# Performance work log

Hardware: AMD Instinct MI355X
Metric: run time of the kernel (lower is better)

Reference implementation:

```python
import jax, jax.numpy as jnp
import numpy as np

N_NODES = 50000
N_EDGES = 800000
D_IN = 96
D_OUT = 96


def setup_inputs() -> dict:
    key = jax.random.key(0)
    k1, k2, k3, k4 = jax.random.split(key, 4)
    feat = jax.random.normal(k1, (N_NODES, D_IN), dtype=jnp.float32)
    # xavier_normal-like init for weight, zeros bias (as in the torch module)
    std = (2.0 / (D_IN + D_OUT)) ** 0.5
    weight = jax.random.normal(k2, (D_IN, D_OUT), dtype=jnp.float32) * std
    bias = jnp.zeros((D_OUT,), dtype=jnp.float32)
    src = jax.random.randint(k3, (N_EDGES,), 0, N_NODES, dtype=jnp.int64)
    dst = jax.random.randint(k4, (N_EDGES,), 0, N_NODES, dtype=jnp.int64)
    return {"feat": feat, "weight": weight, "bias": bias, "src": src, "dst": dst}


def reference(feat, weight, bias, src, dst):
    N = feat.shape[0]
    ones = jnp.ones(src.shape[0], dtype=feat.dtype)
    out_deg = jax.ops.segment_sum(ones, src, num_segments=N)  # out-degree per node
    in_deg = jax.ops.segment_sum(ones, dst, num_segments=N)   # in-degree per node
    ci = jnp.clip(out_deg, 1.0, None) ** -0.5                 # src-side norm
    cj = jnp.clip(in_deg, 1.0, None) ** -0.5                  # dst-side norm
    # gather src features * ci, scatter-sum to dst, scale by cj
    msg = feat[src] * ci[src, None]                           # [E, D_IN]
    agg = jax.ops.segment_sum(msg, dst, num_segments=N) * cj[:, None]
    # DGL UDF reduce only updates nodes that receive messages; isolated
    # (zero in-degree) nodes keep their original features.
    h = jnp.where(in_deg[:, None] > 0, agg, feat)
    return jnp.matmul(h, weight) + bias
```

## Files before the change

kernel.cpp:

```cpp
#include <hip/hip_runtime.h>

#define N_NODES 50000
#define N_EDGES 800000
#define D 96
#define D4 (D / 4)

#define HB 128
#define CHUNK (N_EDGES / HB)
#define NW (N_NODES / 4)

#define RL 12
#define NTILES (N_NODES / 16)
#define CONV_BLOCKS ((N_NODES * RL + 255) / 256)
#define WPREP_BLOCKS ((D * (D / 2) + 255) / 256)

typedef __attribute__((ext_vector_type(8))) short short8;
typedef __attribute__((ext_vector_type(4))) float floatx4;

__device__ __forceinline__ short8 as_short8(uint4 u) { return *(short8*)&u; }

__global__ void __launch_bounds__(1024) hist_kernel(
        const int* __restrict__ src, const int* __restrict__ dst,
        unsigned* __restrict__ hist, unsigned* __restrict__ total) {
    __shared__ unsigned hbin[NW];
    int b = blockIdx.x, t = threadIdx.x;
    if (b == 0 && t == 0) *total = 0;
    int e0 = b * CHUNK;
#pragma unroll 1
    for (int p = 0; p < 2; ++p) {
        const int* __restrict__ arr = (p == 0) ? src : dst;
        for (int i = t; i < NW; i += 1024) hbin[i] = 0;
        __syncthreads();
        for (int i = t; i < CHUNK; i += 1024) {
            int l = arr[e0 + i];
            atomicAdd(&hbin[l >> 2], 1u << ((l & 3) * 8));
        }
        __syncthreads();
        unsigned* __restrict__ g = hist + ((size_t)p * HB + b) * NW;
        for (int i = t; i < NW; i += 1024) g[i] = hbin[i];
        __syncthreads();
    }
}

__global__ void __launch_bounds__(256) reduce_kernel(
        unsigned* __restrict__ hist, float* __restrict__ ci,
        int* __restrict__ deg_in, int* __restrict__ off,
        unsigned* __restrict__ total) {
    int w = blockIdx.x * 256 + threadIdx.x;
    bool valid = w < NW;
    unsigned acc_s = 0;
    int4 dv = {0, 0, 0, 0};
    if (valid) {
        const unsigned* __restrict__ ps = hist + w;
        unsigned* __restrict__ pd = hist + (size_t)HB * NW + w;
#pragma unroll 8
        for (int b = 0; b < HB; ++b) acc_s += ps[(size_t)b * NW];
        unsigned run = 0;
#pragma unroll 4
        for (int b = 0; b < HB; ++b) {
            unsigned v = pd[(size_t)b * NW];
            pd[(size_t)b * NW] = run;
            run += v;
        }
        dv.x = (int)( run        & 0xFFu);
        dv.y = (int)((run >>  8) & 0xFFu);
        dv.z = (int)((run >> 16) & 0xFFu);
        dv.w = (int)( run >> 24        );
    }
    int sum4 = dv.x + dv.y + dv.z + dv.w;
    int lane = threadIdx.x & 63;
    int incl = sum4;
#pragma unroll
    for (int st = 1; st < 64; st <<= 1) {
        int v = __shfl_up(incl, st, 64);
        if (lane >= st) incl += v;
    }
    int excl = incl - sum4;
    int wave_total = __shfl(incl, 63, 64);
    int base = 0;
    if (lane == 63) base = (int)atomicAdd(total, (unsigned)wave_total);
    base = __shfl(base, 63, 64);
    if (valid) {
        int n0 = 4 * w;
        int b0 = base + excl;
        int4 ov;
        ov.x = b0;
        ov.y = b0 + dv.x;
        ov.z = b0 + dv.x + dv.y;
        ov.w = b0 + dv.x + dv.y + dv.z;
        *(int4*)&off[n0] = ov;
        *(int4*)&deg_in[n0] = dv;
        float4 cv;
        cv.x = rsqrtf(fmaxf((float)( acc_s        & 0xFFu), 1.0f));
        cv.y = rsqrtf(fmaxf((float)((acc_s >>  8) & 0xFFu), 1.0f));
        cv.z = rsqrtf(fmaxf((float)((acc_s >> 16) & 0xFFu), 1.0f));
        cv.w = rsqrtf(fmaxf((float)( acc_s >> 24        ), 1.0f));
        *(float4*)&ci[n0] = cv;
    }
}

__device__ __forceinline__ unsigned bf16pack(float a, float b) {
    unsigned ua = __float_as_uint(a);
    unsigned ub = __float_as_uint(b);
    ua = (ua + 0x7FFFu + ((ua >> 16) & 1u)) >> 16;
    ub = (ub + 0x7FFFu + ((ub >> 16) & 1u)) & 0xFFFF0000u;
    return ua | ub;
}

__global__ void __launch_bounds__(256) conv_kernel(
        const float4* __restrict__ feat4, const float* __restrict__ ci,
        uint4* __restrict__ sfeat, const float* __restrict__ W,
        unsigned* __restrict__ WT32) {
    int blk = blockIdx.x;
    if (blk >= CONV_BLOCKS) {
        int t = (blk - CONV_BLOCKS) * 256 + threadIdx.x;
        if (t >= D * (D / 2)) return;
        int n = t / (D / 2);
        int j = t - n * (D / 2);
        float w0 = W[(2 * j) * D + n];
        float w1 = W[(2 * j + 1) * D + n];
        WT32[n * (D / 2) + j] = bf16pack(w0, w1);
        return;
    }
    int t = blk * 256 + threadIdx.x;
    if (t >= N_NODES * RL) return;
    int n = t / RL;
    int lane = t - n * RL;
    float c = ci[n];
    float4 a = feat4[n * D4 + lane * 2];
    float4 b = feat4[n * D4 + lane * 2 + 1];
    uint4 o;
    o.x = bf16pack(a.x * c, a.y * c);
    o.y = bf16pack(a.z * c, a.w * c);
    o.z = bf16pack(b.x * c, b.y * c);
    o.w = bf16pack(b.z * c, b.w * c);
    sfeat[t] = o;
}

__global__ void __launch_bounds__(1024) fill_kernel(
        const int* __restrict__ src, const int* __restrict__ dst,
        const int* __restrict__ off, const unsigned* __restrict__ hist,
        int* __restrict__ csr) {
    __shared__ unsigned cur[NW];
    int b = blockIdx.x, t = threadIdx.x;
    const unsigned* __restrict__ pr = hist + ((size_t)HB + b) * NW;
    for (int i = t; i < NW; i += 1024) cur[i] = pr[i];
    __syncthreads();
    int e0 = b * CHUNK;
    for (int i = t; i < CHUNK; i += 1024) {
        int d = dst[e0 + i];
        int sh = (d & 3) * 8;
        unsigned old = atomicAdd(&cur[d >> 2], 1u << sh);
        int pos = (int)((old >> sh) & 0xFFu);
        csr[off[d] + pos] = src[e0 + i];
    }
}

__global__ void __launch_bounds__(192) gather_kernel(
        const float4* __restrict__ feat4, const uint4* __restrict__ sfeat,
        const int* __restrict__ deg_in, const int* __restrict__ off,
        const int* __restrict__ csr, uint4* __restrict__ hbuf) {
    int tid = threadIdx.x;
    int g = tid / RL;
    int lane = tid - g * RL;
    int n = blockIdx.x * 16 + g;
    int deg = deg_in[n];
    uint4* __restrict__ hout = hbuf + (size_t)n * RL + lane;
    if (deg == 0) {
        float4 a = feat4[n * D4 + lane * 2];
        float4 b = feat4[n * D4 + lane * 2 + 1];
        uint4 o;
        o.x = bf16pack(a.x, a.y);
        o.y = bf16pack(a.z, a.w);
        o.z = bf16pack(b.x, b.y);
        o.w = bf16pack(b.z, b.w);
        *hout = o;
        return;
    }
    const int* bk = csr + off[n];
    const uint4* __restrict__ sf = sfeat + lane;
    float acc[8] = {};
#define ACC8(v)  { \
    acc[0] += __uint_as_float((v).x << 16); \
    acc[1] += __uint_as_float((v).x & 0xFFFF0000u); \
    acc[2] += __uint_as_float((v).y << 16); \
    acc[3] += __uint_as_float((v).y & 0xFFFF0000u); \
    acc[4] += __uint_as_float((v).z << 16); \
    acc[5] += __uint_as_float((v).z & 0xFFFF0000u); \
    acc[6] += __uint_as_float((v).w << 16); \
    acc[7] += __uint_as_float((v).w & 0xFFFF0000u); }
    int i = 0;
    for (; i + 3 < deg; i += 4) {
        int s0 = bk[i], s1 = bk[i + 1], s2 = bk[i + 2], s3 = bk[i + 3];
        uint4 v0 = sf[(size_t)s0 * RL];
        uint4 v1 = sf[(size_t)s1 * RL];
        uint4 v2 = sf[(size_t)s2 * RL];
        uint4 v3 = sf[(size_t)s3 * RL];
        ACC8(v0); ACC8(v1); ACC8(v2); ACC8(v3);
    }
    for (; i < deg; ++i) {
        uint4 v = sf[(size_t)bk[i] * RL];
        ACC8(v);
    }
#undef ACC8
    float cj = rsqrtf((float)deg);
    uint4 o;
    o.x = bf16pack(acc[0] * cj, acc[1] * cj);
    o.y = bf16pack(acc[2] * cj, acc[3] * cj);
    o.z = bf16pack(acc[4] * cj, acc[5] * cj);
    o.w = bf16pack(acc[6] * cj, acc[7] * cj);
    *hout = o;
}

__global__ void __launch_bounds__(256) mfma_mm_kernel(
        const uint4* __restrict__ hb4, const uint4* __restrict__ wt4,
        const float* __restrict__ bias, float* __restrict__ out) {
    int wave = threadIdx.x >> 6;
    int lane = threadIdx.x & 63;
    int tile = blockIdx.x * 4 + wave;
    if (tile >= NTILES) return;
    int m = lane & 15, quad = lane >> 4;
    int row0 = tile * 16;
    int rb = (row0 + m) * RL + quad;
    short8 a0 = as_short8(hb4[rb]);
    short8 a1 = as_short8(hb4[rb + 4]);
    short8 a2 = as_short8(hb4[rb + 8]);
    int r_out0 = row0 + quad * 4;
#pragma unroll
    for (int ct = 0; ct < 6; ++ct) {
        int n = ct * 16 + m;
        int wb = n * RL + quad;
        short8 b0 = as_short8(wt4[wb]);
        short8 b1 = as_short8(wt4[wb + 4]);
        short8 b2 = as_short8(wt4[wb + 8]);
        floatx4 c = {0.f, 0.f, 0.f, 0.f};
        c = __builtin_amdgcn_mfma_f32_16x16x32_bf16(a0, b0, c, 0, 0, 0);
        c = __builtin_amdgcn_mfma_f32_16x16x32_bf16(a1, b1, c, 0, 0, 0);
        c = __builtin_amdgcn_mfma_f32_16x16x32_bf16(a2, b2, c, 0, 0, 0);
        float bs = bias[n];
#pragma unroll
        for (int r = 0; r < 4; ++r)
            out[(size_t)(r_out0 + r) * D + n] = c[r] + bs;
    }
}

extern "C" void kernel_launch(void* const* d_in, const int* in_sizes, int n_in,
                              void* d_out, int out_size, void* d_ws, size_t ws_size,
                              hipStream_t stream) {
    const float* feat = (const float*)d_in[0];
    const float* W    = (const float*)d_in[1];
    const float* bias = (const float*)d_in[2];
    const int*   src  = (const int*)d_in[3];
    const int*   dst  = (const int*)d_in[4];

    unsigned* hist   = (unsigned*)d_ws;
    float*    ci     = (float*)(hist + (size_t)2 * HB * NW);
    int*      off    = (int*)(ci + N_NODES);
    int*      deg_in = off + N_NODES;
    int*      csr    = deg_in + N_NODES;
    uint4*    sfeat  = (uint4*)(csr + N_EDGES);
    uint4*    hbuf   = sfeat + (size_t)N_NODES * RL;
    unsigned* WT32   = (unsigned*)(hbuf + (size_t)N_NODES * RL);
    unsigned* total  = WT32 + D * (D / 2);

    hist_kernel<<<HB, 1024, 0, stream>>>(src, dst, hist, total);
    reduce_kernel<<<(NW + 255) / 256, 256, 0, stream>>>(hist, ci, deg_in, off, total);
    conv_kernel<<<CONV_BLOCKS + WPREP_BLOCKS, 256, 0, stream>>>(
        (const float4*)feat, ci, sfeat, W, WT32);
    fill_kernel<<<HB, 1024, 0, stream>>>(src, dst, off, hist, csr);
    gather_kernel<<<N_NODES / 16, 192, 0, stream>>>(
        (const float4*)feat, sfeat, deg_in, off, csr, hbuf);
    mfma_mm_kernel<<<(NTILES + 3) / 4, 256, 0, stream>>>(
        hbuf, (const uint4*)WT32, bias, (float*)d_out);
}
```

Before: 159.6 us.

## Store CSR source indices as 16-bit with 8-aligned padded segments

Narrows the CSR neighbor-index array from 32-bit to 16-bit and pads each node's segment to a multiple of 8 entries. The gather kernel can then fetch 8 indices with one 16-byte vector load and issue 8 independent feature loads per iteration. The aim is to cut index bandwidth and load count and to raise memory-level parallelism in the gather. However, node ids up to 49999 fit in 16 bits only as unsigned values, and casting src to unsigned short depends on N_NODES staying below 65536.

```diff
diff --git a/kernel.cpp b/kernel.cpp
--- a/kernel.cpp
+++ b/kernel.cpp
@@ -13,6 +13,7 @@
 #define NTILES (N_NODES / 16)
 #define CONV_BLOCKS ((N_NODES * RL + 255) / 256)
 #define WPREP_BLOCKS ((D * (D / 2) + 255) / 256)
+#define CSR_CAP (N_EDGES + 8 * N_NODES)
 
 typedef __attribute__((ext_vector_type(8))) short short8;
 typedef __attribute__((ext_vector_type(4))) float floatx4;
@@ -67,7 +68,12 @@
         dv.z = (int)((run >> 16) & 0xFFu);
         dv.w = (int)( run >> 24        );
     }
-    int sum4 = dv.x + dv.y + dv.z + dv.w;
+    int4 pv;
+    pv.x = (dv.x + 7) & ~7;
+    pv.y = (dv.y + 7) & ~7;
+    pv.z = (dv.z + 7) & ~7;
+    pv.w = (dv.w + 7) & ~7;
+    int sum4 = pv.x + pv.y + pv.z + pv.w;
     int lane = threadIdx.x & 63;
     int incl = sum4;
 #pragma unroll
@@ -85,9 +91,9 @@
         int b0 = base + excl;
         int4 ov;
         ov.x = b0;
-        ov.y = b0 + dv.x;
-        ov.z = b0 + dv.x + dv.y;
-        ov.w = b0 + dv.x + dv.y + dv.z;
+        ov.y = b0 + pv.x;
+        ov.z = b0 + pv.x + pv.y;
+        ov.w = b0 + pv.x + pv.y + pv.z;
         *(int4*)&off[n0] = ov;
         *(int4*)&deg_in[n0] = dv;
         float4 cv;
@@ -140,7 +146,7 @@
 __global__ void __launch_bounds__(1024) fill_kernel(
         const int* __restrict__ src, const int* __restrict__ dst,
         const int* __restrict__ off, const unsigned* __restrict__ hist,
-        int* __restrict__ csr) {
+        unsigned short* __restrict__ csr) {
     __shared__ unsigned cur[NW];
     int b = blockIdx.x, t = threadIdx.x;
     const unsigned* __restrict__ pr = hist + ((size_t)HB + b) * NW;
@@ -152,14 +158,14 @@
         int sh = (d & 3) * 8;
         unsigned old = atomicAdd(&cur[d >> 2], 1u << sh);
         int pos = (int)((old >> sh) & 0xFFu);
-        csr[off[d] + pos] = src[e0 + i];
+        csr[off[d] + pos] = (unsigned short)src[e0 + i];
     }
 }
 
 __global__ void __launch_bounds__(192) gather_kernel(
         const float4* __restrict__ feat4, const uint4* __restrict__ sfeat,
         const int* __restrict__ deg_in, const int* __restrict__ off,
-        const int* __restrict__ csr, uint4* __restrict__ hbuf) {
+        const unsigned short* __restrict__ csr, uint4* __restrict__ hbuf) {
     int tid = threadIdx.x;
     int g = tid / RL;
     int lane = tid - g * RL;
@@ -177,7 +183,7 @@
         *hout = o;
         return;
     }
-    const int* bk = csr + off[n];
+    const unsigned short* __restrict__ bk = csr + off[n];
     const uint4* __restrict__ sf = sfeat + lane;
     float acc[8] = {};
 #define ACC8(v)  { \
@@ -189,14 +195,24 @@
     acc[5] += __uint_as_float((v).z & 0xFFFF0000u); \
     acc[6] += __uint_as_float((v).w << 16); \
     acc[7] += __uint_as_float((v).w & 0xFFFF0000u); }
+    int full = deg & ~7;
     int i = 0;
-    for (; i + 3 < deg; i += 4) {
-        int s0 = bk[i], s1 = bk[i + 1], s2 = bk[i + 2], s3 = bk[i + 3];
+    for (; i < full; i += 8) {
+        uint4 idx = *(const uint4*)(bk + i);
+        unsigned s0 = idx.x & 0xFFFFu, s1 = idx.x >> 16;
+        unsigned s2 = idx.y & 0xFFFFu, s3 = idx.y >> 16;
+        unsigned s4 = idx.z & 0xFFFFu, s5 = idx.z >> 16;
+        unsigned s6 = idx.w & 0xFFFFu, s7 = idx.w >> 16;
         uint4 v0 = sf[(size_t)s0 * RL];
         uint4 v1 = sf[(size_t)s1 * RL];
         uint4 v2 = sf[(size_t)s2 * RL];
         uint4 v3 = sf[(size_t)s3 * RL];
+        uint4 v4 = sf[(size_t)s4 * RL];
+        uint4 v5 = sf[(size_t)s5 * RL];
+        uint4 v6 = sf[(size_t)s6 * RL];
+        uint4 v7 = sf[(size_t)s7 * RL];
         ACC8(v0); ACC8(v1); ACC8(v2); ACC8(v3);
+        ACC8(v4); ACC8(v5); ACC8(v6); ACC8(v7);
     }
     for (; i < deg; ++i) {
         uint4 v = sf[(size_t)bk[i] * RL];
@@ -253,15 +269,15 @@
     const int*   src  = (const int*)d_in[3];
     const int*   dst  = (const int*)d_in[4];
 
-    unsigned* hist   = (unsigned*)d_ws;
-    float*    ci     = (float*)(hist + (size_t)2 * HB * NW);
-    int*      off    = (int*)(ci + N_NODES);
-    int*      deg_in = off + N_NODES;
-    int*      csr    = deg_in + N_NODES;
-    uint4*    sfeat  = (uint4*)(csr + N_EDGES);
-    uint4*    hbuf   = sfeat + (size_t)N_NODES * RL;
-    unsigned* WT32   = (unsigned*)(hbuf + (size_t)N_NODES * RL);
-    unsigned* total  = WT32 + D * (D / 2);
+    unsigned*       hist   = (unsigned*)d_ws;
+    float*          ci     = (float*)(hist + (size_t)2 * HB * NW);
+    int*            off    = (int*)(ci + N_NODES);
+    int*            deg_in = off + N_NODES;
+    unsigned short* csr    = (unsigned short*)(deg_in + N_NODES);
+    uint4*          sfeat  = (uint4*)((char*)csr + ((size_t)CSR_CAP * 2 + 15 & ~15));
+    uint4*          hbuf   = sfeat + (size_t)N_NODES * RL;
+    unsigned*       WT32   = (unsigned*)(hbuf + (size_t)N_NODES * RL);
+    unsigned*       total  = WT32 + D * (D / 2);
 
     hist_kernel<<<HB, 1024, 0, stream>>>(src, dst, hist, total);
     reduce_kernel<<<(NW + 255) / 256, 256, 0, stream>>>(hist, ci, deg_in, off, total);
```

After: 159.7 us. About the same (+0.1%).
